# Optimization experiments

Measured on AMD Instinct MI355X. Metric: run time of the kernel, lower is better.

Reference implementation:

```python
import jax, jax.numpy as jnp
from jax import lax
import numpy as np

NUM_GROUPS = 8
MAX_ITER = 10


def setup_inputs() -> dict:
    key = jax.random.key(0)
    N, deg, q = 50000, 32, NUM_GROUPS
    m = N * deg // 2  # undirected edges
    rng = np.random.default_rng(0)
    u = rng.integers(0, N, m)
    v = (u + 1 + rng.integers(0, N - 1, m)) % N  # no self loops
    src = jnp.asarray(np.concatenate([u, v]), dtype=jnp.int32)  # [E=2m] directed
    dst = jnp.asarray(np.concatenate([v, u]), dtype=jnp.int32)
    k1, k2 = jax.random.split(key)
    msg_init = jax.random.uniform(k1, (2 * m, q), dtype=jnp.float32)
    psi_init = jax.random.uniform(k2, (N, q), dtype=jnp.float32)
    # beta_ast = log(q / (sqrt(c) - 1) + 1), as in __init__ with mean_degree=c
    beta = jnp.log(q / (jnp.sqrt(jnp.float32(deg)) - 1.0) + 1.0)[None]
    return {"msg_init": msg_init, "psi_init": psi_init, "beta": beta,
            "src": src, "dst": dst, "N": N}


def reference(msg_init, psi_init, beta, src, dst, N):
    E = src.shape[0]
    m = E // 2
    q = msg_init.shape[1]
    # reverse-edge index: edge e=(i->j) has reverse rev[e]=(j->i)
    rev = jnp.concatenate([jnp.arange(m, E), jnp.arange(m)])
    mean_w = float(E) / float(N * N)  # W.mean() for unweighted symmetric adjacency
    b = beta[0]
    # normalized random init (init_messages)
    msg = msg_init / msg_init.sum(1, keepdims=True)   # [E, q] message along each directed edge
    psi = psi_init / psi_init.sum(1, keepdims=True)   # [N, q]
    h0 = -b * mean_w * psi.sum(0)                      # [q] external field (init_h)
    ew = jnp.exp(b) - 1.0                              # exp(beta*W_ij)-1 with W_ij=1

    def step(carry, _):
        msg, psi, h = carry
        logterm = jnp.log1p(msg * ew)                                  # [E, q]
        node_in = jax.ops.segment_sum(logterm, dst, num_segments=N)    # [N, q] sum over incoming edges
        # message i->j: product over neighbors k of i except j, times exp(h), normalized
        new_msg = jax.nn.softmax(node_in[src] - logterm[rev] + h, axis=-1)
        # marginal psi_i: product over all neighbors, times exp(h), normalized
        new_psi = jax.nn.softmax(node_in + h, axis=-1)
        new_h = -b * mean_w * new_psi.sum(0)
        return (new_msg, new_psi, new_h), None

    (msg, psi, h), _ = lax.scan(step, (msg, psi, h0), None, length=MAX_ITER)

    u, v = src[:m], dst[:m]  # undirected edge list
    # compute_reg: sum_e W_ij * ||psi_i - psi_j||^2 / m
    reg = jnp.sum((psi[u] - psi[v]) ** 2) / m
    # compute_modularity (argmax assignment, non-differentiable)
    assign = jnp.argmax(psi, axis=1)
    delta = (assign[u] == assign[v]).astype(jnp.float32)
    modularity = jnp.sum(delta * (1.0 - mean_w)) / m
    # entropy loss, scaled by 4*log(1/2)/log(1/q)
    H = -jnp.mean(jnp.sum(psi * jnp.log(psi + 1e-12), axis=1))
    entropy_loss = H * jnp.float32(4.0 * np.log(0.5) / np.log(1.0 / q))
    return psi, reg, entropy_loss, modularity
```

## Files before the change

kernel.cpp:

```cpp
#include <hip/hip_runtime.h>
#include <hip/hip_fp16.h>
#include <math.h>

#define Q 8
#define TPB 256
#define WPB (TPB / 64)
#define SCAN_T 1024

struct alignas(16) H8 { __half h[8]; };


__device__ __forceinline__ float fast_rcp(float x) {
  return __builtin_amdgcn_rcpf(x);
}

__device__ __forceinline__ void load8(const float* __restrict__ p, float r[Q]) {
  const float4* p4 = reinterpret_cast<const float4*>(p);
  float4 a = p4[0], b = p4[1];
  r[0]=a.x; r[1]=a.y; r[2]=a.z; r[3]=a.w;
  r[4]=b.x; r[5]=b.y; r[6]=b.z; r[7]=b.w;
}

__device__ __forceinline__ void store8h(__half* __restrict__ p, const float r[Q]) {
  H8 t;
#pragma unroll
  for (int j=0;j<Q;j++) t.h[j] = __float2half(r[j]);
  *reinterpret_cast<H8*>(p) = t;
}

__device__ __forceinline__ float wave_sum(float x) {
  x += __shfl_down(x, 32);
  x += __shfl_down(x, 16);
  x += __shfl_down(x, 8);
  x += __shfl_down(x, 4);
  x += __shfl_down(x, 2);
  x += __shfl_down(x, 1);
  return x;
}

__device__ __forceinline__ void block_reduce_atomic(float x, float* target, float* lds) {
  float w = wave_sum(x);
  const int lane = threadIdx.x & 63, wid = threadIdx.x >> 6;
  if (lane == 0) lds[wid] = w;
  __syncthreads();
  if (threadIdx.x == 0) {
    float t = 0.f;
#pragma unroll
    for (int i = 0; i < WPB; i++) t += lds[i];
    atomicAdd(target, t);
  }
  __syncthreads();
}

__device__ __forceinline__ float sum8_lanes(float x) {
  x += __shfl_xor(x, 1);
  x += __shfl_xor(x, 2);
  x += __shfl_xor(x, 4);
  return x;
}


__global__ void k_count_pos(const int* __restrict__ dst, int* __restrict__ cnt,
                            int* __restrict__ pos, int E) {
  int i0 = (blockIdx.x * TPB + threadIdx.x) * 4;
  if (i0 + 3 < E) {
    int4 d = *reinterpret_cast<const int4*>(dst + i0);
    int p0 = atomicAdd(&cnt[d.x], 1);
    int p1 = atomicAdd(&cnt[d.y], 1);
    int p2 = atomicAdd(&cnt[d.z], 1);
    int p3 = atomicAdd(&cnt[d.w], 1);
    *reinterpret_cast<int4*>(pos + i0) = make_int4(p0, p1, p2, p3);
  } else {
    for (int e = i0; e < E; e++) pos[e] = atomicAdd(&cnt[dst[e]], 1);
  }
}

__global__ void k_scan1(const int* __restrict__ cnt, int* __restrict__ row_ptr,
                        int* __restrict__ bsum, int N) {
  __shared__ int lds[SCAN_T];
  const int tid = threadIdx.x;
  const int i = blockIdx.x * SCAN_T + tid;
  int c = (i < N) ? cnt[i] : 0;
  lds[tid] = c;
  __syncthreads();
  for (int off = 1; off < SCAN_T; off <<= 1) {
    int v = (tid >= off) ? lds[tid - off] : 0;
    __syncthreads();
    lds[tid] += v;
    __syncthreads();
  }
  if (i < N) row_ptr[i] = lds[tid] - c;
  if (tid == SCAN_T - 1) bsum[blockIdx.x] = lds[tid];
}

__global__ void k_scan2(const int* __restrict__ bsum, int* __restrict__ boffs,
                        int* __restrict__ row_ptr, int nb, int N) {
  __shared__ int lds[SCAN_T];
  const int tid = threadIdx.x;
  int v = (tid < nb) ? bsum[tid] : 0;
  lds[tid] = v;
  __syncthreads();
  for (int off = 1; off < SCAN_T; off <<= 1) {
    int t = (tid >= off) ? lds[tid - off] : 0;
    __syncthreads();
    lds[tid] += t;
    __syncthreads();
  }
  if (tid < nb) boffs[tid] = lds[tid] - v;
  if (tid == 0) row_ptr[N] = lds[nb - 1];
}

__global__ void k_scan3(int* __restrict__ row_ptr, const int* __restrict__ boffs, int N) {
  int i = blockIdx.x * SCAN_T + threadIdx.x;
  if (i < N) row_ptr[i] += boffs[blockIdx.x];
}

__global__ void k_build(const int* __restrict__ src, const int* __restrict__ dst,
                        const int* __restrict__ pos, const int* __restrict__ row_ptr,
                        const float* __restrict__ msg_init,
                        const float* __restrict__ beta,
                        int* __restrict__ rev, __half* __restrict__ t0, int m) {
  int i = blockIdx.x * TPB + threadIdx.x;
  if (i >= m) return;
  const float b  = beta[0];
  const float ew = expf(b) - 1.0f;
  const int u = src[i], v = dst[i];
  const int pu = pos[i] + row_ptr[v];
  const int pv = pos[i + m] + row_ptr[u];
  rev[pu] = pv;
  rev[pv] = pu;

  float r0[Q], r1[Q];
  load8(msg_init + (size_t)i * Q, r0);
  load8(msg_init + ((size_t)i + (size_t)m) * Q, r1);
  float s0 = 0.f, s1 = 0.f;
#pragma unroll
  for (int j=0;j<Q;j++) { s0 += r0[j]; s1 += r1[j]; }
  float i0 = ew / s0, i1 = ew / s1;
#pragma unroll
  for (int j=0;j<Q;j++) { r0[j] = fmaf(r0[j], i0, 1.0f); r1[j] = fmaf(r1[j], i1, 1.0f); }
  store8h(t0 + (size_t)pu * Q, r0);
  store8h(t0 + (size_t)pv * Q, r1);
}


__global__ void k_pi0cav(const int* __restrict__ row_ptr, const __half* __restrict__ t0,
                         __half* __restrict__ cav0, float* __restrict__ pi0, int N) {
  const int tid = threadIdx.x;
  const int s = tid & 7;
  const int u = (blockIdx.x * TPB + tid) >> 3;
  if (u >= N) return;
  const int st = row_ptr[u], en = row_ptr[u + 1];
  float prod[Q];
#pragma unroll
  for (int j=0;j<Q;j++) prod[j] = 1.f;
  for (int r = st + s; r < en; r += 8) {
    H8 t = *reinterpret_cast<const H8*>(t0 + (size_t)r * Q);
#pragma unroll
    for (int j=0;j<Q;j++) prod[j] *= __half2float(t.h[j]);
  }
#pragma unroll
  for (int j=0;j<Q;j++) {
    prod[j] *= __shfl_xor(prod[j], 1);
    prod[j] *= __shfl_xor(prod[j], 2);
    prod[j] *= __shfl_xor(prod[j], 4);
  }
  if (s == 0) {
    float4* o = reinterpret_cast<float4*>(pi0 + (size_t)u * Q);
    o[0] = make_float4(prod[0], prod[1], prod[2], prod[3]);
    o[1] = make_float4(prod[4], prod[5], prod[6], prod[7]);
  }
  for (int r = st + s; r < en; r += 8) {
    H8 t = *reinterpret_cast<const H8*>(t0 + (size_t)r * Q);
    float c[Q]; float sm = 0.f;
#pragma unroll
    for (int j=0;j<Q;j++) { c[j] = prod[j] * fast_rcp(__half2float(t.h[j])); sm += c[j]; }
    float inv = fast_rcp(sm);
    H8 o;
#pragma unroll
    for (int j=0;j<Q;j++) o.h[j] = __float2half(c[j] * inv);
    *reinterpret_cast<H8*>(cav0 + (size_t)r * Q) = o;
  }
}

__global__ void k_init_nodes(const float* __restrict__ psi_init,
                             float* __restrict__ S0, int N) {
  __shared__ float lds[WPB];
  int n = blockIdx.x * TPB + threadIdx.x;
  float p[Q];
  if (n < N) {
    load8(psi_init + (size_t)n * Q, p);
    float s = 0.f;
#pragma unroll
    for (int j=0;j<Q;j++) s += p[j];
    float inv = 1.0f / s;
#pragma unroll
    for (int j=0;j<Q;j++) p[j] *= inv;
  } else {
#pragma unroll
    for (int j=0;j<Q;j++) p[j] = 0.f;
  }
#pragma unroll
  for (int j=0;j<Q;j++) {
    block_reduce_atomic(p[j], &S0[j], lds);
  }
}

__global__ void k_iter2(const int* __restrict__ row_ptr,
                        const int* __restrict__ rev,
                        const __half* __restrict__ cavIn,
                        __half* __restrict__ cavOut,
                        const float* __restrict__ pi_cur,
                        float* __restrict__ pi_nxt,
                        const float* __restrict__ beta,
                        const float* __restrict__ S,
                        float* __restrict__ S_nxt,
                        float neg_mw, int N, int writeCav) {
  __shared__ float part[WPB][Q];
  const int tid = threadIdx.x;
  const int s = tid & 7;
  const float b  = beta[0];
  const float ew = expf(b) - 1.0f;
  const float hb = neg_mw * b;
  float eh[Q];
#pragma unroll
  for (int j=0;j<Q;j++) eh[j] = expf(hb * S[j]);
  const float ehs = expf(hb * S[s]);
  float sacc = 0.f;

  const int u = (blockIdx.x * TPB + tid) >> 3;
  if (u < N) {
    const int st = row_ptr[u], en = row_ptr[u + 1];
    float prod[Q];
#pragma unroll
    for (int j=0;j<Q;j++) prod[j] = 1.f;
    for (int r = st + s; r < en; r += 8) {
      const int rv = rev[r];
      H8 c = *reinterpret_cast<const H8*>(cavIn + (size_t)rv * Q);
      float num[Q]; float sm = 0.f;
#pragma unroll
      for (int j=0;j<Q;j++) { num[j] = eh[j] * __half2float(c.h[j]); sm += num[j]; }
      const float inv = fast_rcp(sm) * ew;
      H8 o;
#pragma unroll
      for (int j=0;j<Q;j++) {
        float tn = fmaf(num[j], inv, 1.0f);
        prod[j] *= tn;
        o.h[j] = __float2half(tn);
      }
      *reinterpret_cast<H8*>(cavOut + (size_t)r * Q) = o;
    }
#pragma unroll
    for (int j=0;j<Q;j++) {
      prod[j] *= __shfl_xor(prod[j], 1);
      prod[j] *= __shfl_xor(prod[j], 2);
      prod[j] *= __shfl_xor(prod[j], 4);
    }
    if (s == 0) {
      float4* o = reinterpret_cast<float4*>(pi_nxt + (size_t)u * Q);
      o[0] = make_float4(prod[0], prod[1], prod[2], prod[3]);
      o[1] = make_float4(prod[4], prod[5], prod[6], prod[7]);
    }
    {
      float pn = pi_cur[(size_t)u * Q + s] * ehs;
      float smp = sum8_lanes(pn);
      sacc = pn * fast_rcp(smp);
    }
    if (writeCav) {
      for (int r = st + s; r < en; r += 8) {
        H8 t = *reinterpret_cast<const H8*>(cavOut + (size_t)r * Q);
        float c[Q]; float sm = 0.f;
#pragma unroll
        for (int j=0;j<Q;j++) { c[j] = prod[j] * fast_rcp(__half2float(t.h[j])); sm += c[j]; }
        const float inv = fast_rcp(sm);
        H8 o;
#pragma unroll
        for (int j=0;j<Q;j++) o.h[j] = __float2half(c[j] * inv);
        *reinterpret_cast<H8*>(cavOut + (size_t)r * Q) = o;
      }
    }
  }
  sacc += __shfl_xor(sacc, 8);
  sacc += __shfl_xor(sacc, 16);
  sacc += __shfl_xor(sacc, 32);
  const int lane = tid & 63, wid = tid >> 6;
  if (lane < Q) part[wid][lane] = sacc;
  __syncthreads();
  if (tid < Q) {
    float tot = 0.f;
#pragma unroll
    for (int w = 0; w < WPB; w++) tot += part[w][tid];
    atomicAdd(&S_nxt[tid], tot);
  }
}


__global__ void k_psi_ent(const float* __restrict__ pi,
                          const float* __restrict__ beta,
                          const float* __restrict__ S,
                          float neg_mw, float* __restrict__ psi,
                          float* __restrict__ H_acc, int N) {
  __shared__ float lds[WPB];
  const int j = threadIdx.x & 7;
  const float eh = expf(neg_mw * beta[0] * S[j]);
  float hacc = 0.f;
  const int g0 = (blockIdx.x * TPB + threadIdx.x) >> 3;
  const int gs = (gridDim.x * TPB) >> 3;
  for (int n = g0; n < N; n += gs) {
    float pn = pi[(size_t)n * Q + j] * eh;
    float p = pn / sum8_lanes(pn);
    psi[(size_t)n * Q + j] = p;
    float el = p * logf(p + 1e-12f);
    el = sum8_lanes(el);
    if (j == 0) hacc += el;
  }
  block_reduce_atomic(hacc, H_acc, lds);
}

__global__ void k_edge_stats(const float* __restrict__ psi,
                             const int* __restrict__ src,
                             const int* __restrict__ dst,
                             float* __restrict__ reg_acc,
                             float* __restrict__ mod_acc,
                             float one_minus_mw, int m) {
  __shared__ float lds1[WPB];
  __shared__ float lds2[WPB];
  float reg = 0.f, mod = 0.f;
  for (int i = blockIdx.x * TPB + threadIdx.x; i < m; i += gridDim.x * TPB) {
    int u = src[i], v = dst[i];
    float pu[Q], pv[Q];
    load8(psi + (size_t)u * Q, pu);
    load8(psi + (size_t)v * Q, pv);
#pragma unroll
    for (int j=0;j<Q;j++) { float d = pu[j] - pv[j]; reg += d * d; }
    int au = 0, av = 0;
    float mu = pu[0], mv = pv[0];
#pragma unroll
    for (int j=1;j<Q;j++) {
      if (pu[j] > mu) { mu = pu[j]; au = j; }
      if (pv[j] > mv) { mv = pv[j]; av = j; }
    }
    if (au == av) mod += one_minus_mw;
  }
  block_reduce_atomic(reg, reg_acc, lds1);
  block_reduce_atomic(mod, mod_acc, lds2);
}

__global__ void k_finalize(const float* __restrict__ H_acc,
                           const float* __restrict__ reg_acc,
                           const float* __restrict__ mod_acc,
                           float* __restrict__ out3,
                           float inv_m, float inv_N, float entc) {
  out3[0] = reg_acc[0] * inv_m;
  out3[1] = (-H_acc[0] * inv_N) * entc;
  out3[2] = mod_acc[0] * inv_m;
}


extern "C" void kernel_launch(void* const* d_in, const int* in_sizes, int n_in,
                              void* d_out, int out_size, void* d_ws, size_t ws_size,
                              hipStream_t stream) {
  const float* msg_init = (const float*)d_in[0];
  const float* psi_init = (const float*)d_in[1];
  const float* beta     = (const float*)d_in[2];
  const int*   src      = (const int*)d_in[3];
  const int*   dst      = (const int*)d_in[4];

  const int E = in_sizes[3];
  const int m = E / 2;
  const int N = in_sizes[1] / Q;
  const double mean_w = (double)E / ((double)N * (double)N);
  const float  neg_mw = (float)(-mean_w);

  float* out = (float*)d_out;

  __half* cavA = (__half*)d_ws;
  __half* cavB = cavA + (size_t)E * Q;
  int*   rev     = (int*)(cavB + (size_t)E * Q);
  int*   pos     = rev + E;
  int*   row_ptr = pos + E;
  int*   cnt     = row_ptr + (N + 1);
  int*   bsum    = cnt + N;
  int*   boffs   = bsum + SCAN_T;
  float* pi0     = (float*)(boffs + SCAN_T);
  float* pi1     = pi0 + (size_t)N * Q;
  float* S       = pi1 + (size_t)N * Q;
  float* H_acc   = S + 11 * Q;
  float* reg_acc = H_acc + 1;
  float* mod_acc = H_acc + 2;

  const int gridC = (E + TPB * 4 - 1) / (TPB * 4);
  const int gridM = (m + TPB - 1) / TPB;
  const int gridN = (N + TPB - 1) / TPB;
  const int gridG = (N * Q + TPB - 1) / TPB;
  const int gridS = min(512, gridM);
  const int nb    = (N + SCAN_T - 1) / SCAN_T;

  const float entc  = (float)(4.0 * log(0.5) / log(1.0 / (double)Q));
  const float inv_m = (float)(1.0 / (double)m);
  const float inv_N = (float)(1.0 / (double)N);
  const float omw   = (float)(1.0 - mean_w);

  hipMemsetAsync(cnt, 0, (size_t)N * sizeof(int), stream);
  hipMemsetAsync(S, 0, (size_t)(11 * Q + 3) * sizeof(float), stream);

  k_count_pos<<<gridC, TPB, 0, stream>>>(dst, cnt, pos, E);
  k_scan1<<<nb, SCAN_T, 0, stream>>>(cnt, row_ptr, bsum, N);
  k_scan2<<<1, SCAN_T, 0, stream>>>(bsum, boffs, row_ptr, nb, N);
  k_scan3<<<nb, SCAN_T, 0, stream>>>(row_ptr, boffs, N);
  k_build<<<gridM, TPB, 0, stream>>>(src, dst, pos, row_ptr, msg_init, beta,
                                     rev, cavB, m);
  k_pi0cav<<<gridG, TPB, 0, stream>>>(row_ptr, cavB, cavA, pi0, N);
  k_init_nodes<<<gridN, TPB, 0, stream>>>(psi_init, S, N);

  __half* ccur = cavA; __half* cnxt = cavB;
  float*  pcur = pi0;  float*  pnxt = pi1;
  for (int t = 0; t < 9; ++t) {
    k_iter2<<<gridG, TPB, 0, stream>>>(row_ptr, rev, ccur, cnxt, pcur, pnxt,
                                       beta, S + t * Q, S + (t + 1) * Q,
                                       neg_mw, N, (t < 8) ? 1 : 0);
    __half* ch = ccur; ccur = cnxt; cnxt = ch;
    float*  pf = pcur; pcur = pnxt; pnxt = pf;
  }

  k_psi_ent<<<gridN, TPB, 0, stream>>>(pcur, beta, S + 9 * Q, neg_mw, out, H_acc, N);
  k_edge_stats<<<gridS, TPB, 0, stream>>>(out, src, dst, reg_acc, mod_acc, omw, m);
  k_finalize<<<1, 1, 0, stream>>>(H_acc, reg_acc, mod_acc, out + (size_t)N * Q,
                                  inv_m, inv_N, entc);
}
```

Before: 740.6 us.

## Split build scatter from t0 init, prefetch gathers in CSR loops

The build kernel now scatters only (reverse index, original edge id) pairs. A separate coalesced kernel computes the initial log-terms in original edge order. The first-pass kernel gathers t0 through the edge id and writes the rev array as it goes, which removes the scattered fp16 stores. The per-node loops in the first-pass and iteration kernels also software-prefetch the next rev/cavity load to hide gather latency. Each count_pos thread now handles 8 edges instead of 4. In exchange the workspace grows by an extra E*Q halves plus E int2, and there is one more launch.

```diff
diff --git a/kernel.cpp b/kernel.cpp
--- a/kernel.cpp
+++ b/kernel.cpp
@@ -19,13 +19,6 @@
   float4 a = p4[0], b = p4[1];
   r[0]=a.x; r[1]=a.y; r[2]=a.z; r[3]=a.w;
   r[4]=b.x; r[5]=b.y; r[6]=b.z; r[7]=b.w;
-}
-
-__device__ __forceinline__ void store8h(__half* __restrict__ p, const float r[Q]) {
-  H8 t;
-#pragma unroll
-  for (int j=0;j<Q;j++) t.h[j] = __float2half(r[j]);
-  *reinterpret_cast<H8*>(p) = t;
 }
 
 __device__ __forceinline__ float wave_sum(float x) {
@@ -62,14 +55,20 @@
 
 __global__ void k_count_pos(const int* __restrict__ dst, int* __restrict__ cnt,
                             int* __restrict__ pos, int E) {
-  int i0 = (blockIdx.x * TPB + threadIdx.x) * 4;
-  if (i0 + 3 < E) {
-    int4 d = *reinterpret_cast<const int4*>(dst + i0);
-    int p0 = atomicAdd(&cnt[d.x], 1);
-    int p1 = atomicAdd(&cnt[d.y], 1);
-    int p2 = atomicAdd(&cnt[d.z], 1);
-    int p3 = atomicAdd(&cnt[d.w], 1);
-    *reinterpret_cast<int4*>(pos + i0) = make_int4(p0, p1, p2, p3);
+  int i0 = (blockIdx.x * TPB + threadIdx.x) * 8;
+  if (i0 + 7 < E) {
+    int4 d0 = *reinterpret_cast<const int4*>(dst + i0);
+    int4 d1 = *reinterpret_cast<const int4*>(dst + i0 + 4);
+    int p0 = atomicAdd(&cnt[d0.x], 1);
+    int p1 = atomicAdd(&cnt[d0.y], 1);
+    int p2 = atomicAdd(&cnt[d0.z], 1);
+    int p3 = atomicAdd(&cnt[d0.w], 1);
+    int p4 = atomicAdd(&cnt[d1.x], 1);
+    int p5 = atomicAdd(&cnt[d1.y], 1);
+    int p6 = atomicAdd(&cnt[d1.z], 1);
+    int p7 = atomicAdd(&cnt[d1.w], 1);
+    *reinterpret_cast<int4*>(pos + i0)     = make_int4(p0, p1, p2, p3);
+    *reinterpret_cast<int4*>(pos + i0 + 4) = make_int4(p4, p5, p6, p7);
   } else {
     for (int e = i0; e < E; e++) pos[e] = atomicAdd(&cnt[dst[e]], 1);
   }
@@ -117,34 +116,39 @@
 
 __global__ void k_build(const int* __restrict__ src, const int* __restrict__ dst,
                         const int* __restrict__ pos, const int* __restrict__ row_ptr,
-                        const float* __restrict__ msg_init,
-                        const float* __restrict__ beta,
-                        int* __restrict__ rev, __half* __restrict__ t0, int m) {
+                        int2* __restrict__ rev_eid, int m) {
   int i = blockIdx.x * TPB + threadIdx.x;
   if (i >= m) return;
-  const float b  = beta[0];
-  const float ew = expf(b) - 1.0f;
   const int u = src[i], v = dst[i];
   const int pu = pos[i] + row_ptr[v];
   const int pv = pos[i + m] + row_ptr[u];
-  rev[pu] = pv;
-  rev[pv] = pu;
-
-  float r0[Q], r1[Q];
-  load8(msg_init + (size_t)i * Q, r0);
-  load8(msg_init + ((size_t)i + (size_t)m) * Q, r1);
-  float s0 = 0.f, s1 = 0.f;
-#pragma unroll
-  for (int j=0;j<Q;j++) { s0 += r0[j]; s1 += r1[j]; }
-  float i0 = ew / s0, i1 = ew / s1;
-#pragma unroll
-  for (int j=0;j<Q;j++) { r0[j] = fmaf(r0[j], i0, 1.0f); r1[j] = fmaf(r1[j], i1, 1.0f); }
-  store8h(t0 + (size_t)pu * Q, r0);
-  store8h(t0 + (size_t)pv * Q, r1);
-}
-
-
-__global__ void k_pi0cav(const int* __restrict__ row_ptr, const __half* __restrict__ t0,
+  rev_eid[pu] = make_int2(pv, i);
+  rev_eid[pv] = make_int2(pu, i + m);
+}
+
+__global__ void k_init_t0(const float* __restrict__ msg_init,
+                          const float* __restrict__ beta,
+                          __half* __restrict__ t0e, int E) {
+  int e = blockIdx.x * TPB + threadIdx.x;
+  if (e >= E) return;
+  const float ew = expf(beta[0]) - 1.0f;
+  float r[Q];
+  load8(msg_init + (size_t)e * Q, r);
+  float s = 0.f;
+#pragma unroll
+  for (int j=0;j<Q;j++) s += r[j];
+  float inv = ew / s;
+  H8 o;
+#pragma unroll
+  for (int j=0;j<Q;j++) o.h[j] = __float2half(fmaf(r[j], inv, 1.0f));
+  *reinterpret_cast<H8*>(t0e + (size_t)e * Q) = o;
+}
+
+
+__global__ void k_pi0cav(const int* __restrict__ row_ptr,
+                         const int2* __restrict__ rev_eid,
+                         const __half* __restrict__ t0e,
+                         int* __restrict__ rev,
                          __half* __restrict__ cav0, float* __restrict__ pi0, int N) {
   const int tid = threadIdx.x;
   const int s = tid & 7;
@@ -154,10 +158,22 @@
   float prod[Q];
 #pragma unroll
   for (int j=0;j<Q;j++) prod[j] = 1.f;
-  for (int r = st + s; r < en; r += 8) {
-    H8 t = *reinterpret_cast<const H8*>(t0 + (size_t)r * Q);
+
+  int r = st + s;
+  int2 re; H8 t;
+  if (r < en) {
+    re = rev_eid[r];
+    t = *reinterpret_cast<const H8*>(t0e + (size_t)re.y * Q);
+  }
+  while (r < en) {
+    const int r2 = r + 8;
+    const int rp = (r2 < en) ? r2 : r;
+    int2 re2 = rev_eid[rp];
+    H8 t2 = *reinterpret_cast<const H8*>(t0e + (size_t)re2.y * Q);
+    rev[r] = re.x;
 #pragma unroll
     for (int j=0;j<Q;j++) prod[j] *= __half2float(t.h[j]);
+    r = r2; re = re2; t = t2;
   }
 #pragma unroll
   for (int j=0;j<Q;j++) {
@@ -170,16 +186,17 @@
     o[0] = make_float4(prod[0], prod[1], prod[2], prod[3]);
     o[1] = make_float4(prod[4], prod[5], prod[6], prod[7]);
   }
-  for (int r = st + s; r < en; r += 8) {
-    H8 t = *reinterpret_cast<const H8*>(t0 + (size_t)r * Q);
+  for (int r2 = st + s; r2 < en; r2 += 8) {
+    int2 re2 = rev_eid[r2];
+    H8 t2 = *reinterpret_cast<const H8*>(t0e + (size_t)re2.y * Q);
     float c[Q]; float sm = 0.f;
 #pragma unroll
-    for (int j=0;j<Q;j++) { c[j] = prod[j] * fast_rcp(__half2float(t.h[j])); sm += c[j]; }
+    for (int j=0;j<Q;j++) { c[j] = prod[j] * fast_rcp(__half2float(t2.h[j])); sm += c[j]; }
     float inv = fast_rcp(sm);
     H8 o;
 #pragma unroll
     for (int j=0;j<Q;j++) o.h[j] = __float2half(c[j] * inv);
-    *reinterpret_cast<H8*>(cav0 + (size_t)r * Q) = o;
+    *reinterpret_cast<H8*>(cav0 + (size_t)r2 * Q) = o;
   }
 }
 
@@ -234,9 +251,18 @@
     float prod[Q];
 #pragma unroll
     for (int j=0;j<Q;j++) prod[j] = 1.f;
-    for (int r = st + s; r < en; r += 8) {
+
+    int r = st + s;
+    H8 c;
+    if (r < en) {
       const int rv = rev[r];
-      H8 c = *reinterpret_cast<const H8*>(cavIn + (size_t)rv * Q);
+      c = *reinterpret_cast<const H8*>(cavIn + (size_t)rv * Q);
+    }
+    while (r < en) {
+      const int r2 = r + 8;
+      const int rp = (r2 < en) ? r2 : r;
+      const int rv2 = rev[rp];
+      H8 c2 = *reinterpret_cast<const H8*>(cavIn + (size_t)rv2 * Q);
       float num[Q]; float sm = 0.f;
 #pragma unroll
       for (int j=0;j<Q;j++) { num[j] = eh[j] * __half2float(c.h[j]); sm += num[j]; }
@@ -249,6 +275,7 @@
         o.h[j] = __float2half(tn);
       }
       *reinterpret_cast<H8*>(cavOut + (size_t)r * Q) = o;
+      r = r2; c = c2;
     }
 #pragma unroll
     for (int j=0;j<Q;j++) {
@@ -267,16 +294,16 @@
       sacc = pn * fast_rcp(smp);
     }
     if (writeCav) {
-      for (int r = st + s; r < en; r += 8) {
-        H8 t = *reinterpret_cast<const H8*>(cavOut + (size_t)r * Q);
-        float c[Q]; float sm = 0.f;
-#pragma unroll
-        for (int j=0;j<Q;j++) { c[j] = prod[j] * fast_rcp(__half2float(t.h[j])); sm += c[j]; }
+      for (int r2 = st + s; r2 < en; r2 += 8) {
+        H8 t = *reinterpret_cast<const H8*>(cavOut + (size_t)r2 * Q);
+        float c2[Q]; float sm = 0.f;
+#pragma unroll
+        for (int j=0;j<Q;j++) { c2[j] = prod[j] * fast_rcp(__half2float(t.h[j])); sm += c2[j]; }
         const float inv = fast_rcp(sm);
         H8 o;
 #pragma unroll
-        for (int j=0;j<Q;j++) o.h[j] = __float2half(c[j] * inv);
-        *reinterpret_cast<H8*>(cavOut + (size_t)r * Q) = o;
+        for (int j=0;j<Q;j++) o.h[j] = __float2half(c2[j] * inv);
+        *reinterpret_cast<H8*>(cavOut + (size_t)r2 * Q) = o;
       }
     }
   }
@@ -376,7 +403,9 @@
 
   __half* cavA = (__half*)d_ws;
   __half* cavB = cavA + (size_t)E * Q;
-  int*   rev     = (int*)(cavB + (size_t)E * Q);
+  __half* t0e  = cavB + (size_t)E * Q;
+  int2*  rev_eid = (int2*)(t0e + (size_t)E * Q);
+  int*   rev     = (int*)(rev_eid + E);
   int*   pos     = rev + E;
   int*   row_ptr = pos + E;
   int*   cnt     = row_ptr + (N + 1);
@@ -389,7 +418,8 @@
   float* reg_acc = H_acc + 1;
   float* mod_acc = H_acc + 2;
 
-  const int gridC = (E + TPB * 4 - 1) / (TPB * 4);
+  const int gridC = (E + TPB * 8 - 1) / (TPB * 8);
+  const int gridE = (E + TPB - 1) / TPB;
   const int gridM = (m + TPB - 1) / TPB;
   const int gridN = (N + TPB - 1) / TPB;
   const int gridG = (N * Q + TPB - 1) / TPB;
@@ -408,9 +438,9 @@
   k_scan1<<<nb, SCAN_T, 0, stream>>>(cnt, row_ptr, bsum, N);
   k_scan2<<<1, SCAN_T, 0, stream>>>(bsum, boffs, row_ptr, nb, N);
   k_scan3<<<nb, SCAN_T, 0, stream>>>(row_ptr, boffs, N);
-  k_build<<<gridM, TPB, 0, stream>>>(src, dst, pos, row_ptr, msg_init, beta,
-                                     rev, cavB, m);
-  k_pi0cav<<<gridG, TPB, 0, stream>>>(row_ptr, cavB, cavA, pi0, N);
+  k_build<<<gridM, TPB, 0, stream>>>(src, dst, pos, row_ptr, rev_eid, m);
+  k_init_t0<<<gridE, TPB, 0, stream>>>(msg_init, beta, t0e, E);
+  k_pi0cav<<<gridG, TPB, 0, stream>>>(row_ptr, rev_eid, t0e, rev, cavA, pi0, N);
   k_init_nodes<<<gridN, TPB, 0, stream>>>(psi_init, S, N);
 
   __half* ccur = cavA; __half* cnxt = cavB;
```

Result: slower. 839.9 us (+13.4%).

## Compute cavity on the fly from neighbor product instead of materializing cavity array

Applied to the files above, without the earlier changes.

Instead of writing normalized cavity messages in a second pass over each node's edges, the iteration now stores only the per-edge log1p terms and recomputes each cavity as pi[src]/t[rev] when it is consumed. The reverse index is packed with the source node into an int2, so one load fetches both, and the next edge's loads are prefetched in software. This drops the second edge loop and its read-modify-write of the half-precision edge array. In exchange it adds a random 32-byte gather of the source node's product per edge and extra reciprocals.

```diff
diff --git a/kernel.cpp b/kernel.cpp
--- a/kernel.cpp
+++ b/kernel.cpp
@@ -119,7 +119,7 @@
                         const int* __restrict__ pos, const int* __restrict__ row_ptr,
                         const float* __restrict__ msg_init,
                         const float* __restrict__ beta,
-                        int* __restrict__ rev, __half* __restrict__ t0, int m) {
+                        int2* __restrict__ rn, __half* __restrict__ t0, int m) {
   int i = blockIdx.x * TPB + threadIdx.x;
   if (i >= m) return;
   const float b  = beta[0];
@@ -127,8 +127,8 @@
   const int u = src[i], v = dst[i];
   const int pu = pos[i] + row_ptr[v];
   const int pv = pos[i + m] + row_ptr[u];
-  rev[pu] = pv;
-  rev[pv] = pu;
+  rn[pu] = make_int2(pv, u);
+  rn[pv] = make_int2(pu, v);
 
   float r0[Q], r1[Q];
   load8(msg_init + (size_t)i * Q, r0);
@@ -144,8 +144,8 @@
 }
 
 
-__global__ void k_pi0cav(const int* __restrict__ row_ptr, const __half* __restrict__ t0,
-                         __half* __restrict__ cav0, float* __restrict__ pi0, int N) {
+__global__ void k_pi0(const int* __restrict__ row_ptr, const __half* __restrict__ t0,
+                      float* __restrict__ pi0, int N) {
   const int tid = threadIdx.x;
   const int s = tid & 7;
   const int u = (blockIdx.x * TPB + tid) >> 3;
@@ -169,17 +169,6 @@
     float4* o = reinterpret_cast<float4*>(pi0 + (size_t)u * Q);
     o[0] = make_float4(prod[0], prod[1], prod[2], prod[3]);
     o[1] = make_float4(prod[4], prod[5], prod[6], prod[7]);
-  }
-  for (int r = st + s; r < en; r += 8) {
-    H8 t = *reinterpret_cast<const H8*>(t0 + (size_t)r * Q);
-    float c[Q]; float sm = 0.f;
-#pragma unroll
-    for (int j=0;j<Q;j++) { c[j] = prod[j] * fast_rcp(__half2float(t.h[j])); sm += c[j]; }
-    float inv = fast_rcp(sm);
-    H8 o;
-#pragma unroll
-    for (int j=0;j<Q;j++) o.h[j] = __float2half(c[j] * inv);
-    *reinterpret_cast<H8*>(cav0 + (size_t)r * Q) = o;
   }
 }
 
@@ -206,16 +195,16 @@
   }
 }
 
-__global__ void k_iter2(const int* __restrict__ row_ptr,
-                        const int* __restrict__ rev,
-                        const __half* __restrict__ cavIn,
-                        __half* __restrict__ cavOut,
+__global__ void k_iter3(const int* __restrict__ row_ptr,
+                        const int2* __restrict__ rn,
+                        const __half* __restrict__ tIn,
+                        __half* __restrict__ tOut,
                         const float* __restrict__ pi_cur,
                         float* __restrict__ pi_nxt,
                         const float* __restrict__ beta,
                         const float* __restrict__ S,
                         float* __restrict__ S_nxt,
-                        float neg_mw, int N, int writeCav) {
+                        float neg_mw, int N, int writeT) {
   __shared__ float part[WPB][Q];
   const int tid = threadIdx.x;
   const int s = tid & 7;
@@ -234,12 +223,33 @@
     float prod[Q];
 #pragma unroll
     for (int j=0;j<Q;j++) prod[j] = 1.f;
-    for (int r = st + s; r < en; r += 8) {
-      const int rv = rev[r];
-      H8 c = *reinterpret_cast<const H8*>(cavIn + (size_t)rv * Q);
+
+    int r = st + s;
+    H8 c; float4 pa, pb;
+    if (r < en) {
+      const int2 w = rn[r];
+      c  = *reinterpret_cast<const H8*>(tIn + (size_t)w.x * Q);
+      const float4* pp = reinterpret_cast<const float4*>(pi_cur + (size_t)w.y * Q);
+      pa = pp[0]; pb = pp[1];
+    }
+    while (r < en) {
+      const int r2 = r + 8;
+      H8 c2; float4 pa2, pb2;
+      if (r2 < en) {
+        const int2 w2 = rn[r2];
+        c2 = *reinterpret_cast<const H8*>(tIn + (size_t)w2.x * Q);
+        const float4* pp2 = reinterpret_cast<const float4*>(pi_cur + (size_t)w2.y * Q);
+        pa2 = pp2[0]; pb2 = pp2[1];
+      }
+      float pv[Q];
+      pv[0]=pa.x; pv[1]=pa.y; pv[2]=pa.z; pv[3]=pa.w;
+      pv[4]=pb.x; pv[5]=pb.y; pv[6]=pb.z; pv[7]=pb.w;
       float num[Q]; float sm = 0.f;
 #pragma unroll
-      for (int j=0;j<Q;j++) { num[j] = eh[j] * __half2float(c.h[j]); sm += num[j]; }
+      for (int j=0;j<Q;j++) {
+        num[j] = eh[j] * pv[j] * fast_rcp(__half2float(c.h[j]));
+        sm += num[j];
+      }
       const float inv = fast_rcp(sm) * ew;
       H8 o;
 #pragma unroll
@@ -248,7 +258,8 @@
         prod[j] *= tn;
         o.h[j] = __float2half(tn);
       }
-      *reinterpret_cast<H8*>(cavOut + (size_t)r * Q) = o;
+      if (writeT) *reinterpret_cast<H8*>(tOut + (size_t)r * Q) = o;
+      r = r2; c = c2; pa = pa2; pb = pb2;
     }
 #pragma unroll
     for (int j=0;j<Q;j++) {
@@ -265,19 +276,6 @@
       float pn = pi_cur[(size_t)u * Q + s] * ehs;
       float smp = sum8_lanes(pn);
       sacc = pn * fast_rcp(smp);
-    }
-    if (writeCav) {
-      for (int r = st + s; r < en; r += 8) {
-        H8 t = *reinterpret_cast<const H8*>(cavOut + (size_t)r * Q);
-        float c[Q]; float sm = 0.f;
-#pragma unroll
-        for (int j=0;j<Q;j++) { c[j] = prod[j] * fast_rcp(__half2float(t.h[j])); sm += c[j]; }
-        const float inv = fast_rcp(sm);
-        H8 o;
-#pragma unroll
-        for (int j=0;j<Q;j++) o.h[j] = __float2half(c[j] * inv);
-        *reinterpret_cast<H8*>(cavOut + (size_t)r * Q) = o;
-      }
     }
   }
   sacc += __shfl_xor(sacc, 8);
@@ -374,10 +372,10 @@
 
   float* out = (float*)d_out;
 
-  __half* cavA = (__half*)d_ws;
-  __half* cavB = cavA + (size_t)E * Q;
-  int*   rev     = (int*)(cavB + (size_t)E * Q);
-  int*   pos     = rev + E;
+  __half* tA = (__half*)d_ws;
+  __half* tB = tA + (size_t)E * Q;
+  int2*  rn      = (int2*)(tB + (size_t)E * Q);
+  int*   pos     = (int*)(rn + E);
   int*   row_ptr = pos + E;
   int*   cnt     = row_ptr + (N + 1);
   int*   bsum    = cnt + N;
@@ -409,17 +407,17 @@
   k_scan2<<<1, SCAN_T, 0, stream>>>(bsum, boffs, row_ptr, nb, N);
   k_scan3<<<nb, SCAN_T, 0, stream>>>(row_ptr, boffs, N);
   k_build<<<gridM, TPB, 0, stream>>>(src, dst, pos, row_ptr, msg_init, beta,
-                                     rev, cavB, m);
-  k_pi0cav<<<gridG, TPB, 0, stream>>>(row_ptr, cavB, cavA, pi0, N);
+                                     rn, tA, m);
+  k_pi0<<<gridG, TPB, 0, stream>>>(row_ptr, tA, pi0, N);
   k_init_nodes<<<gridN, TPB, 0, stream>>>(psi_init, S, N);
 
-  __half* ccur = cavA; __half* cnxt = cavB;
-  float*  pcur = pi0;  float*  pnxt = pi1;
+  __half* tcur = tA; __half* tnxt = tB;
+  float*  pcur = pi0; float* pnxt = pi1;
   for (int t = 0; t < 9; ++t) {
-    k_iter2<<<gridG, TPB, 0, stream>>>(row_ptr, rev, ccur, cnxt, pcur, pnxt,
+    k_iter3<<<gridG, TPB, 0, stream>>>(row_ptr, rn, tcur, tnxt, pcur, pnxt,
                                        beta, S + t * Q, S + (t + 1) * Q,
                                        neg_mw, N, (t < 8) ? 1 : 0);
-    __half* ch = ccur; ccur = cnxt; cnxt = ch;
+    __half* th = tcur; tcur = tnxt; tnxt = th;
     float*  pf = pcur; pcur = pnxt; pnxt = pf;
   }
 
```

New measurement: 697.7 us. 5.8% less time.
